# Kernel tuning notes

Measured on AMD Instinct MI355X. Metric: run time of the kernel, lower is better.

Reference implementation:

```python
import jax, jax.numpy as jnp
import numpy as np

DIM = 2048
NUM_HEADS = 16
HEAD_DIM = 128
MAX_SEQ_LEN = 2048
ATTN_SCALE = 0.12
EPS = 1e-6


def _rms_norm(x):
    # RMSNorm without learned weight, over last dim
    return x * jax.lax.rsqrt(jnp.mean(jnp.square(x), axis=-1, keepdims=True) + EPS)


def _rope_tables(T):
    # half of the head dim rotates, half is identity (zero frequency)
    quarter = HEAD_DIM // 4
    angular_freq = (1.0 / 1024.0) ** jnp.linspace(0.0, 1.0, quarter, dtype=jnp.float32)
    angular_freq = jnp.concatenate([angular_freq, jnp.zeros(quarter, dtype=jnp.float32)])  # [D/2]
    t = jnp.arange(T, dtype=jnp.float32)
    theta = t[:, None] * angular_freq[None, :]  # [T, D/2]
    return jnp.cos(theta), jnp.sin(theta)


def _apply_rope(x, cos, sin):
    # x: [B, T, H, D]; cos/sin: [T, D/2] -> broadcast [1, T, 1, D/2]
    x1, x2 = jnp.split(x, 2, axis=-1)
    c = cos[None, :, None, :]
    s = sin[None, :, None, :]
    y1 = x1 * c + x2 * s
    y2 = -x1 * s + x2 * c
    return jnp.concatenate([y1, y2], axis=-1)


def setup_inputs() -> dict:
    key = jax.random.key(0)
    k1, k2, k3, k4 = jax.random.split(key, 4)
    hdim = NUM_HEADS * HEAD_DIM
    x = jax.random.normal(k1, (1, MAX_SEQ_LEN, DIM), dtype=jnp.float32)
    qkvo_w = jax.random.normal(k2, (4, hdim, DIM), dtype=jnp.float32) * (DIM ** -0.5)
    ve = jax.random.normal(k3, (1, MAX_SEQ_LEN, hdim), dtype=jnp.float32)
    lambdas = jax.random.uniform(k4, (2,), dtype=jnp.float32)
    return {"x": x, "qkvo_w": qkvo_w, "ve": ve, "lambdas": lambdas}


def reference(x, qkvo_w, ve, lambdas):
    B, T, _ = x.shape
    H, D = NUM_HEADS, HEAD_DIM
    # fused qkv projection: [B, T, 3*H*D]
    qkv = jnp.einsum('btc,ehc->bteh', x, qkvo_w[:3]).reshape(B, T, 3, H, D)
    q, k, v = qkv[:, :, 0], qkv[:, :, 1], qkv[:, :, 2]  # each [B, T, H, D]
    q, k, v = _rms_norm(q), _rms_norm(k), _rms_norm(v)
    cos, sin = _rope_tables(T)
    q = _apply_rope(q, cos, sin)
    k = _apply_rope(k, cos, sin)
    v = lambdas[0] * v + lambdas[1] * ve.reshape(B, T, H, D)
    # causal attention with fixed scale
    scores = jnp.einsum('bthd,bshd->bhts', q, k) * ATTN_SCALE  # [B, H, T, T]
    causal = jnp.tril(jnp.ones((T, T), dtype=bool))
    scores = jnp.where(causal[None, None], scores, -jnp.inf)
    p = jax.nn.softmax(scores, axis=-1)
    y = jnp.einsum('bhts,bshd->bthd', p, v).reshape(B, T, H * D)
    return jnp.einsum('bth,ch->btc', y, qkvo_w[3])
```

## Files before the change

kernel.cpp:

```cpp
#include <hip/hip_runtime.h>
#include <math.h>

#define SEQ  2048
#define CDIM 2048
#define NH   16
#define DH   128
#define HDIM 2048

typedef __attribute__((ext_vector_type(8))) short  bf16x8;
typedef __attribute__((ext_vector_type(4))) float  f32x4;
typedef unsigned short ushort_t;

__device__ __forceinline__ unsigned short f2bf(float f) {
  unsigned u = __float_as_uint(f);
  u = (u + 0x7fffu + ((u >> 16) & 1u)) >> 16;
  return (unsigned short)u;
}
__device__ __forceinline__ float b2f(unsigned short s) {
  return __uint_as_float((unsigned)s << 16);
}

__device__ __forceinline__ void async_ld16(const ushort_t* g, ushort_t* l) {
  __builtin_amdgcn_global_load_lds((const __attribute__((address_space(1))) unsigned int*)g,
                                   (__attribute__((address_space(3))) unsigned int*)l,
                                   16, 0, 0);
}

__device__ __forceinline__ f32x4 mfma16(bf16x8 a, bf16x8 b, f32x4 c) {
  return __builtin_amdgcn_mfma_f32_16x16x32_bf16(a, b, c, 0, 0, 0);
}

__global__ __launch_bounds__(256) void to_bf16(const float* __restrict__ src,
                                               ushort_t* __restrict__ dst, int n8) {
  int i = blockIdx.x * 256 + threadIdx.x;
  if (i >= n8) return;
  const float4* s = (const float4*)src;
  float4 f0 = s[i * 2], f1 = s[i * 2 + 1];
  bf16x8 o;
  o[0] = (short)f2bf(f0.x); o[1] = (short)f2bf(f0.y);
  o[2] = (short)f2bf(f0.z); o[3] = (short)f2bf(f0.w);
  o[4] = (short)f2bf(f1.x); o[5] = (short)f2bf(f1.y);
  o[6] = (short)f2bf(f1.z); o[7] = (short)f2bf(f1.w);
  *(bf16x8*)&dst[i * 8] = o;
}

template <int OUT_BF16>
__global__ __launch_bounds__(256) void gemm_bf16(const ushort_t* __restrict__ A,
                                                 const ushort_t* __restrict__ B,
                                                 void* __restrict__ Cv,
                                                 long bStride, long cStride) {
  constexpr int K = CDIM, N = HDIM;
  __shared__ __align__(16) ushort_t As[2][128 * 32];
  __shared__ __align__(16) ushort_t Bs[2][128 * 32];
  const ushort_t* Bp = B + (long)blockIdx.z * bStride;
  const int m0 = blockIdx.y * 128, n0 = blockIdx.x * 128;
  const int tid = threadIdx.x, lane = tid & 63, wave = tid >> 6;
  const int wm = wave >> 1, wn = wave & 1;
  const int g = lane >> 4, l15 = lane & 15;
  const int srow = tid >> 2, scc = tid & 3;

  f32x4 acc[4][4];
#pragma unroll
  for (int i = 0; i < 4; ++i)
#pragma unroll
    for (int j = 0; j < 4; ++j) acc[i][j] = (f32x4)0.0f;

  auto stage = [&](int buf, int k0) {
    int r0 = srow, r1 = srow + 64;
    int c0 = scc ^ ((r0 >> 1) & 3), c1 = scc ^ ((r1 >> 1) & 3);
    async_ld16(&A [(long)(m0 + r0) * K + k0 + c0 * 8], &As[buf][wave * 512]);
    async_ld16(&A [(long)(m0 + r1) * K + k0 + c1 * 8], &As[buf][2048 + wave * 512]);
    async_ld16(&Bp[(long)(n0 + r0) * K + k0 + c0 * 8], &Bs[buf][wave * 512]);
    async_ld16(&Bp[(long)(n0 + r1) * K + k0 + c1 * 8], &Bs[buf][2048 + wave * 512]);
  };

  stage(0, 0);
  int cur = 0;
  for (int k0 = 0; k0 < K; k0 += 32) {
    __syncthreads();
    if (k0 + 32 < K) stage(cur ^ 1, k0 + 32);

    bf16x8 af[4], bfr[4];
#pragma unroll
    for (int mi = 0; mi < 4; ++mi) {
      int row = wm * 64 + mi * 16 + l15;
      int cc = g ^ ((row >> 1) & 3);
      af[mi] = *(const bf16x8*)&As[cur][row * 32 + cc * 8];
    }
#pragma unroll
    for (int ni = 0; ni < 4; ++ni) {
      int row = wn * 64 + ni * 16 + l15;
      int cc = g ^ ((row >> 1) & 3);
      bfr[ni] = *(const bf16x8*)&Bs[cur][row * 32 + cc * 8];
    }
#pragma unroll
    for (int mi = 0; mi < 4; ++mi)
#pragma unroll
      for (int ni = 0; ni < 4; ++ni)
        acc[mi][ni] = mfma16(af[mi], bfr[ni], acc[mi][ni]);
    cur ^= 1;
  }

#pragma unroll
  for (int mi = 0; mi < 4; ++mi)
#pragma unroll
    for (int ni = 0; ni < 4; ++ni) {
      int row = m0 + wm * 64 + mi * 16 + g * 4;
      int col = n0 + wn * 64 + ni * 16 + l15;
#pragma unroll
      for (int r = 0; r < 4; ++r) {
        if (OUT_BF16)
          ((ushort_t*)Cv)[cStride * blockIdx.z + (long)(row + r) * N + col] = f2bf(acc[mi][ni][r]);
        else
          ((float*)Cv)[(long)(row + r) * N + col] = acc[mi][ni][r];
      }
    }
}

__device__ __forceinline__ float wave_sum64(float x) {
#pragma unroll
  for (int m = 32; m >= 1; m >>= 1) x += __shfl_xor(x, m, 64);
  return x;
}

__global__ __launch_bounds__(256) void norm_rope(ushort_t* __restrict__ qkvb,
                                                 const float* __restrict__ ve,
                                                 const float* __restrict__ lambdas) {
  const int gid = blockIdx.x * 4 + (threadIdx.x >> 6);
  const int t = gid >> 4, h = gid & 15;
  const int d = threadIdx.x & 63;
  const long base = (long)t * HDIM + h * DH;
  ushort_t* q = qkvb + base;
  ushort_t* k = qkvb + (long)SEQ * HDIM + base;
  ushort_t* v = qkvb + 2L * SEQ * HDIM + base;

  float q1 = b2f(q[d]), q2 = b2f(q[d + 64]);
  float k1 = b2f(k[d]), k2 = b2f(k[d + 64]);
  float v1 = b2f(v[d]), v2 = b2f(v[d + 64]);

  float qsc = rsqrtf(wave_sum64(q1 * q1 + q2 * q2) * (1.0f / 128.0f) + 1e-6f);
  float ksc = rsqrtf(wave_sum64(k1 * k1 + k2 * k2) * (1.0f / 128.0f) + 1e-6f);
  float vsc = rsqrtf(wave_sum64(v1 * v1 + v2 * v2) * (1.0f / 128.0f) + 1e-6f);
  q1 *= qsc; q2 *= qsc;
  k1 *= ksc; k2 *= ksc;
  v1 *= vsc; v2 *= vsc;

  float freq = (d < 32) ? powf(1.0f / 1024.0f, (float)d * (1.0f / 31.0f)) : 0.0f;
  float th = (float)t * freq;
  float c = cosf(th), s = sinf(th);

  float qo1 = q1 * c + q2 * s, qo2 = -q1 * s + q2 * c;
  float ko1 = k1 * c + k2 * s, ko2 = -k1 * s + k2 * c;

  float l0 = lambdas[0], l1 = lambdas[1];
  const float* vep = ve + base;
  float vo1 = l0 * v1 + l1 * vep[d];
  float vo2 = l0 * v2 + l1 * vep[d + 64];

  q[d] = f2bf(qo1); q[d + 64] = f2bf(qo2);
  k[d] = f2bf(ko1); k[d + 64] = f2bf(ko2);
  v[d] = f2bf(vo1); v[d + 64] = f2bf(vo2);
}

__global__ __launch_bounds__(256) void transpose_v(const ushort_t* __restrict__ vb,
                                                   ushort_t* __restrict__ vbT) {
  __shared__ __align__(16) ushort_t L[64 * 136];
  const int t0 = blockIdx.x * 64, h = blockIdx.y;
  const int tid = threadIdx.x;
#pragma unroll
  for (int p = 0; p < 4; ++p) {
    int idx = p * 256 + tid;
    int row = idx >> 4, cc = idx & 15;
    *(bf16x8*)&L[row * 136 + cc * 8] =
        *(const bf16x8*)&vb[(long)(t0 + row) * HDIM + h * DH + cc * 8];
  }
  __syncthreads();
#pragma unroll
  for (int p = 0; p < 4; ++p) {
    int idx = p * 256 + tid;
    int d = idx >> 3, tc = (idx & 7) * 8;
    bf16x8 o;
#pragma unroll
    for (int j = 0; j < 8; ++j) o[j] = (short)L[(tc + j) * 136 + d];
    *(bf16x8*)&vbT[((long)h * DH + d) * SEQ + t0 + tc] = o;
  }
}

__global__ __launch_bounds__(256) void flash_mfma(const ushort_t* __restrict__ qkvb,
                                                  const ushort_t* __restrict__ vbT,
                                                  ushort_t* __restrict__ yb) {
  __shared__ __align__(16) ushort_t Ks[2][64 * 128];
  __shared__ __align__(16) ushort_t Vt[2][128 * 64];
  __shared__ __align__(16) ushort_t Ps[64 * 72];
  const int h = blockIdx.y;
  const int qi = (h < 8) ? blockIdx.x : (31 - blockIdx.x);
  const int q0 = qi * 64;
  const int tid = threadIdx.x, lane = tid & 63, wave = tid >> 6;
  const int g = lane >> 4, l15 = lane & 15;
  const ushort_t* Kg = qkvb + (long)SEQ * HDIM;
  const ushort_t* Vg = vbT + (long)h * DH * SEQ;

  bf16x8 qf[4];
#pragma unroll
  for (int ks = 0; ks < 4; ++ks)
    qf[ks] = *(const bf16x8*)
        &qkvb[(long)(q0 + wave * 16 + l15) * HDIM + h * DH + ks * 32 + g * 8];

  f32x4 oacc[8];
#pragma unroll
  for (int dt = 0; dt < 8; ++dt) oacc[dt] = (f32x4)0.0f;
  float mrow = -1e30f, lrow = 0.0f;

  auto stage = [&](int buf, int s0) {
#pragma unroll
    for (int i = 0; i < 4; ++i) {
      int idx = i * 256 + tid;
      { int row = idx >> 4, cc = idx & 15, cg = cc ^ (row & 7);
        async_ld16(&Kg[(long)(s0 + row) * HDIM + h * DH + cg * 8],
                   &Ks[buf][i * 2048 + wave * 512]); }
      { int row = idx >> 3, cc = idx & 7,  cg = cc ^ (row & 7);
        async_ld16(&Vg[(long)row * SEQ + s0 + cg * 8],
                   &Vt[buf][i * 2048 + wave * 512]); }
    }
  };

  stage(0, 0);
  int cur = 0;
  for (int s0 = 0; s0 <= q0; s0 += 64) {
    __syncthreads();
    if (s0 + 64 <= q0) stage(cur ^ 1, s0 + 64);

    f32x4 st[4];
#pragma unroll
    for (int mt = 0; mt < 4; ++mt) st[mt] = (f32x4)0.0f;
    __builtin_amdgcn_s_setprio(1);
#pragma unroll
    for (int ks = 0; ks < 4; ++ks)
#pragma unroll
      for (int mt = 0; mt < 4; ++mt) {
        int row = mt * 16 + l15;
        int cc = (ks * 4 + g) ^ (row & 7);
        bf16x8 a = *(const bf16x8*)&Ks[cur][row * 128 + cc * 8];
        st[mt] = mfma16(a, qf[ks], st[mt]);
      }
    __builtin_amdgcn_s_setprio(0);

    const int qg = q0 + wave * 16 + l15;
    float p[4][4];
#pragma unroll
    for (int mt = 0; mt < 4; ++mt)
#pragma unroll
      for (int r = 0; r < 4; ++r) p[mt][r] = st[mt][r] * 0.12f;
    if (s0 == q0) {
#pragma unroll
      for (int mt = 0; mt < 4; ++mt)
#pragma unroll
        for (int r = 0; r < 4; ++r)
          if (s0 + mt * 16 + g * 4 + r > qg) p[mt][r] = -1e30f;
    }
    float tmax = -1e30f;
#pragma unroll
    for (int mt = 0; mt < 4; ++mt)
#pragma unroll
      for (int r = 0; r < 4; ++r) tmax = fmaxf(tmax, p[mt][r]);
    tmax = fmaxf(tmax, __shfl_xor(tmax, 16, 64));
    tmax = fmaxf(tmax, __shfl_xor(tmax, 32, 64));
    float nm = fmaxf(mrow, tmax);
    float alpha = __expf(mrow - nm);
    float psum = 0.0f;
#pragma unroll
    for (int mt = 0; mt < 4; ++mt) {
      float e0 = __expf(p[mt][0] - nm), e1 = __expf(p[mt][1] - nm);
      float e2 = __expf(p[mt][2] - nm), e3 = __expf(p[mt][3] - nm);
      unsigned short b0 = f2bf(e0), b1 = f2bf(e1), b2 = f2bf(e2), b3 = f2bf(e3);
      psum += b2f(b0) + b2f(b1) + b2f(b2) + b2f(b3);
      unsigned lo = (unsigned)b0 | ((unsigned)b1 << 16);
      unsigned hi = (unsigned)b2 | ((unsigned)b3 << 16);
      *(uint2*)&Ps[(wave * 16 + l15) * 72 + mt * 16 + g * 4] = make_uint2(lo, hi);
    }
    psum += __shfl_xor(psum, 16, 64);
    psum += __shfl_xor(psum, 32, 64);
    mrow = nm;
    lrow = lrow * alpha + psum;

    float aO[4];
#pragma unroll
    for (int r = 0; r < 4; ++r) aO[r] = __shfl(alpha, g * 4 + r, 64);
#pragma unroll
    for (int dt = 0; dt < 8; ++dt)
#pragma unroll
      for (int r = 0; r < 4; ++r) oacc[dt][r] *= aO[r];

    __builtin_amdgcn_s_setprio(1);
#pragma unroll
    for (int ks = 0; ks < 2; ++ks) {
      bf16x8 ap = *(const bf16x8*)&Ps[(wave * 16 + l15) * 72 + ks * 32 + g * 8];
#pragma unroll
      for (int dt = 0; dt < 8; ++dt) {
        int row = dt * 16 + l15;
        int cc = (ks * 4 + g) ^ (row & 7);
        bf16x8 bv = *(const bf16x8*)&Vt[cur][row * 64 + cc * 8];
        oacc[dt] = mfma16(ap, bv, oacc[dt]);
      }
    }
    __builtin_amdgcn_s_setprio(0);
    cur ^= 1;
  }

  float linv[4];
#pragma unroll
  for (int r = 0; r < 4; ++r) linv[r] = 1.0f / __shfl(lrow, g * 4 + r, 64);
#pragma unroll
  for (int dt = 0; dt < 8; ++dt) {
    int row = q0 + wave * 16 + g * 4;
    int col = h * DH + dt * 16 + l15;
#pragma unroll
    for (int r = 0; r < 4; ++r)
      yb[(long)(row + r) * HDIM + col] = f2bf(oacc[dt][r] * linv[r]);
  }
}

extern "C" void kernel_launch(void* const* d_in, const int* in_sizes, int n_in,
                              void* d_out, int out_size, void* d_ws, size_t ws_size,
                              hipStream_t stream) {
  const float* x       = (const float*)d_in[0];
  const float* w       = (const float*)d_in[1];
  const float* ve      = (const float*)d_in[2];
  const float* lambdas = (const float*)d_in[3];
  float* out = (float*)d_out;

  char* ws = (char*)d_ws;
  ushort_t* qkvb = (ushort_t*)ws;
  ushort_t* xb   = (ushort_t*)(ws + 25165824);
  ushort_t* wb   = (ushort_t*)(ws + 33554432);
  ushort_t* vbT  = (ushort_t*)(ws + 67108864);
  ushort_t* yb   = xb;

  to_bf16<<<2048, 256, 0, stream>>>(x, xb, (SEQ * CDIM) / 8);
  to_bf16<<<8192, 256, 0, stream>>>(w, wb, (4 * HDIM * CDIM) / 8);
  gemm_bf16<1><<<dim3(16, 16, 3), 256, 0, stream>>>(xb, wb, qkvb,
                                                    (long)HDIM * CDIM, (long)SEQ * HDIM);
  norm_rope<<<(SEQ * NH) / 4, 256, 0, stream>>>(qkvb, ve, lambdas);
  transpose_v<<<dim3(SEQ / 64, NH), 256, 0, stream>>>(qkvb + 2L * SEQ * HDIM, vbT);
  flash_mfma<<<dim3(SEQ / 64, NH), 256, 0, stream>>>(qkvb, vbT, yb);
  gemm_bf16<0><<<dim3(16, 16, 1), 256, 0, stream>>>(yb, wb + 3L * HDIM * CDIM, out, 0, 0);
}
```

Before: 321.9 us.

## Keep P in registers via transposed PV MFMA and merge bf16 conversion launches

The flash attention kernel computes the transposed output O^T = V^T P^T, so the softmax probabilities stay in registers as the B operand and no longer round-trip through the Ps shared-memory buffer. It also drops the alpha/l cross-lane shuffles and writes output as packed 8-byte stores. In exchange, V fragments are now assembled from two 8-byte LDS reads per MFMA. Separately, the two fp32-to-bf16 conversion kernels are merged into one launch.

Result: no change. 321.7 us (-0.1%).

```diff
diff --git a/kernel.cpp b/kernel.cpp
--- a/kernel.cpp
+++ b/kernel.cpp
@@ -30,18 +30,28 @@
   return __builtin_amdgcn_mfma_f32_16x16x32_bf16(a, b, c, 0, 0, 0);
 }
 
-__global__ __launch_bounds__(256) void to_bf16(const float* __restrict__ src,
-                                               ushort_t* __restrict__ dst, int n8) {
+__global__ __launch_bounds__(256) void to_bf16_2(const float* __restrict__ s1,
+                                                 ushort_t* __restrict__ d1, int n1,
+                                                 const float* __restrict__ s2,
+                                                 ushort_t* __restrict__ d2, int n2) {
   int i = blockIdx.x * 256 + threadIdx.x;
-  if (i >= n8) return;
-  const float4* s = (const float4*)src;
-  float4 f0 = s[i * 2], f1 = s[i * 2 + 1];
+  const float* s;
+  ushort_t* d;
+  int j;
+  if (i < n1) { s = s1; d = d1; j = i; }
+  else {
+    j = i - n1;
+    if (j >= n2) return;
+    s = s2; d = d2;
+  }
+  const float4* sp = (const float4*)s;
+  float4 f0 = sp[j * 2], f1 = sp[j * 2 + 1];
   bf16x8 o;
   o[0] = (short)f2bf(f0.x); o[1] = (short)f2bf(f0.y);
   o[2] = (short)f2bf(f0.z); o[3] = (short)f2bf(f0.w);
   o[4] = (short)f2bf(f1.x); o[5] = (short)f2bf(f1.y);
   o[6] = (short)f2bf(f1.z); o[7] = (short)f2bf(f1.w);
-  *(bf16x8*)&dst[i * 8] = o;
+  *(bf16x8*)&d[j * 8] = o;
 }
 
 template <int OUT_BF16>
@@ -191,7 +201,6 @@
                                                   ushort_t* __restrict__ yb) {
   __shared__ __align__(16) ushort_t Ks[2][64 * 128];
   __shared__ __align__(16) ushort_t Vt[2][128 * 64];
-  __shared__ __align__(16) ushort_t Ps[64 * 72];
   const int h = blockIdx.y;
   const int qi = (h < 8) ? blockIdx.x : (31 - blockIdx.x);
   const int q0 = qi * 64;
@@ -206,9 +215,9 @@
     qf[ks] = *(const bf16x8*)
         &qkvb[(long)(q0 + wave * 16 + l15) * HDIM + h * DH + ks * 32 + g * 8];
 
-  f32x4 oacc[8];
-#pragma unroll
-  for (int dt = 0; dt < 8; ++dt) oacc[dt] = (f32x4)0.0f;
+  f32x4 oaccT[8];
+#pragma unroll
+  for (int dt = 0; dt < 8; ++dt) oaccT[dt] = (f32x4)0.0f;
   float mrow = -1e30f, lrow = 0.0f;
 
   auto stage = [&](int buf, int s0) {
@@ -268,55 +277,58 @@
     float nm = fmaxf(mrow, tmax);
     float alpha = __expf(mrow - nm);
     float psum = 0.0f;
+    unsigned plo[4], phi[4];
 #pragma unroll
     for (int mt = 0; mt < 4; ++mt) {
       float e0 = __expf(p[mt][0] - nm), e1 = __expf(p[mt][1] - nm);
       float e2 = __expf(p[mt][2] - nm), e3 = __expf(p[mt][3] - nm);
       unsigned short b0 = f2bf(e0), b1 = f2bf(e1), b2 = f2bf(e2), b3 = f2bf(e3);
       psum += b2f(b0) + b2f(b1) + b2f(b2) + b2f(b3);
-      unsigned lo = (unsigned)b0 | ((unsigned)b1 << 16);
-      unsigned hi = (unsigned)b2 | ((unsigned)b3 << 16);
-      *(uint2*)&Ps[(wave * 16 + l15) * 72 + mt * 16 + g * 4] = make_uint2(lo, hi);
+      plo[mt] = (unsigned)b0 | ((unsigned)b1 << 16);
+      phi[mt] = (unsigned)b2 | ((unsigned)b3 << 16);
     }
     psum += __shfl_xor(psum, 16, 64);
     psum += __shfl_xor(psum, 32, 64);
     mrow = nm;
     lrow = lrow * alpha + psum;
 
-    float aO[4];
-#pragma unroll
-    for (int r = 0; r < 4; ++r) aO[r] = __shfl(alpha, g * 4 + r, 64);
 #pragma unroll
     for (int dt = 0; dt < 8; ++dt)
 #pragma unroll
-      for (int r = 0; r < 4; ++r) oacc[dt][r] *= aO[r];
+      for (int r = 0; r < 4; ++r) oaccT[dt][r] *= alpha;
 
     __builtin_amdgcn_s_setprio(1);
 #pragma unroll
     for (int ks = 0; ks < 2; ++ks) {
-      bf16x8 ap = *(const bf16x8*)&Ps[(wave * 16 + l15) * 72 + ks * 32 + g * 8];
+      uint4 pw = make_uint4(plo[ks * 2], phi[ks * 2], plo[ks * 2 + 1], phi[ks * 2 + 1]);
+      bf16x8 pfr = *(bf16x8*)&pw;
 #pragma unroll
       for (int dt = 0; dt < 8; ++dt) {
         int row = dt * 16 + l15;
-        int cc = (ks * 4 + g) ^ (row & 7);
-        bf16x8 bv = *(const bf16x8*)&Vt[cur][row * 64 + cc * 8];
-        oacc[dt] = mfma16(ap, bv, oacc[dt]);
+        int cA = (ks * 4 + (g >> 1)) ^ (row & 7);
+        int cB = (ks * 4 + 2 + (g >> 1)) ^ (row & 7);
+        const ushort_t* vrow = &Vt[cur][row * 64];
+        uint2 va = *(const uint2*)&vrow[cA * 8 + (g & 1) * 4];
+        uint2 vb = *(const uint2*)&vrow[cB * 8 + (g & 1) * 4];
+        uint4 vw = make_uint4(va.x, va.y, vb.x, vb.y);
+        bf16x8 av = *(bf16x8*)&vw;
+        oaccT[dt] = mfma16(av, pfr, oaccT[dt]);
       }
     }
     __builtin_amdgcn_s_setprio(0);
     cur ^= 1;
   }
 
-  float linv[4];
-#pragma unroll
-  for (int r = 0; r < 4; ++r) linv[r] = 1.0f / __shfl(lrow, g * 4 + r, 64);
+  float linv = 1.0f / lrow;
+  const long row = q0 + wave * 16 + l15;
 #pragma unroll
   for (int dt = 0; dt < 8; ++dt) {
-    int row = q0 + wave * 16 + g * 4;
-    int col = h * DH + dt * 16 + l15;
-#pragma unroll
-    for (int r = 0; r < 4; ++r)
-      yb[(long)(row + r) * HDIM + col] = f2bf(oacc[dt][r] * linv[r]);
+    int col = h * DH + dt * 16 + g * 4;
+    unsigned w0 = (unsigned)f2bf(oaccT[dt][0] * linv) |
+                  ((unsigned)f2bf(oaccT[dt][1] * linv) << 16);
+    unsigned w1 = (unsigned)f2bf(oaccT[dt][2] * linv) |
+                  ((unsigned)f2bf(oaccT[dt][3] * linv) << 16);
+    *(uint2*)&yb[row * HDIM + col] = make_uint2(w0, w1);
   }
 }
 
@@ -336,8 +348,8 @@
   ushort_t* vbT  = (ushort_t*)(ws + 67108864);
   ushort_t* yb   = xb;
 
-  to_bf16<<<2048, 256, 0, stream>>>(x, xb, (SEQ * CDIM) / 8);
-  to_bf16<<<8192, 256, 0, stream>>>(w, wb, (4 * HDIM * CDIM) / 8);
+  const int n1 = (SEQ * CDIM) / 8, n2 = (4 * HDIM * CDIM) / 8;
+  to_bf16_2<<<(n1 + n2 + 255) / 256, 256, 0, stream>>>(x, xb, n1, w, wb, n2);
   gemm_bf16<1><<<dim3(16, 16, 3), 256, 0, stream>>>(xb, wb, qkvb,
                                                     (long)HDIM * CDIM, (long)SEQ * HDIM);
   norm_rope<<<(SEQ * NH) / 4, 256, 0, stream>>>(qkvb, ve, lambdas);
```
